# Kernel optimization log

Hardware: AMD Instinct MI355X
Metric: run time of the kernel (lower is better)

## Reference

```python
import jax, jax.numpy as jnp
import numpy as np

D_MODEL = 1024
N_HEADS = 16
D_HEAD = D_MODEL // N_HEADS


def setup_inputs() -> dict:
    key = jax.random.key(0)
    k1, k2, k3 = jax.random.split(key, 3)
    x = jax.random.normal(k1, (4, 2048, D_MODEL), dtype=jnp.float32)
    # nn.Linear weights stored [out, in]; we keep that convention.
    s = 1.0 / np.sqrt(D_MODEL)
    W_qkv = jax.random.uniform(k2, (3 * D_MODEL, D_MODEL), dtype=jnp.float32, minval=-s, maxval=s)
    W_out = jax.random.uniform(k3, (D_MODEL, D_MODEL), dtype=jnp.float32, minval=-s, maxval=s)
    return {"x": x, "W_qkv": W_qkv, "W_out": W_out}


def reference(x, W_qkv, W_out):
    B, T, C = x.shape
    qkv = jnp.einsum('btc,oc->bto', x, W_qkv)  # [B,T,3C]
    q, k, v = jnp.split(qkv, 3, axis=-1)

    def split_heads(t):
        return t.reshape(B, T, N_HEADS, D_HEAD).transpose(0, 2, 1, 3)  # [B,H,T,Dh]

    q, k, v = split_heads(q), split_heads(k), split_heads(v)
    scale = D_HEAD ** -0.5
    scores = jnp.einsum('bhqd,bhkd->bhqk', q, k) * scale  # [B,H,T,T]
    mask = jnp.triu(jnp.ones((T, T), dtype=bool), k=1)
    scores = jnp.where(mask, -jnp.inf, scores)
    att = jax.nn.softmax(scores, axis=-1)
    out = jnp.einsum('bhqk,bhkd->bhqd', att, v)
    out = out.transpose(0, 2, 1, 3).reshape(B, T, C)
    return jnp.einsum('btc,oc->bto', out, W_out)
```

## Files before the change

### kernel.cpp

```cpp
#include <hip/hip_runtime.h>
#include <hip/hip_bf16.h>
#include <math.h>


typedef __attribute__((ext_vector_type(8))) short bf16x8;
typedef __attribute__((ext_vector_type(4))) float f32x4;

__device__ __forceinline__ void async16(const void* g, void* l) {
    __builtin_amdgcn_global_load_lds((const __attribute__((address_space(1))) void*)g,
                                     (__attribute__((address_space(3))) void*)l,
                                     16, 0, 0);
}

__device__ __forceinline__ unsigned short f2b(float f) {
    __hip_bfloat16 h = __float2bfloat16(f);
    return *(unsigned short*)&h;
}

__device__ __forceinline__ unsigned int packbf2(float a, float b) {
    __hip_bfloat162 h2 = __float22bfloat162_rn(make_float2(a, b));
    return *(unsigned int*)&h2;
}

__global__ __launch_bounds__(256)
void cast3_f32_bf16(const float* __restrict__ a, unsigned short* __restrict__ oa, int na,
                    const float* __restrict__ b, unsigned short* __restrict__ ob, int nb,
                    const float* __restrict__ c, unsigned short* __restrict__ oc, int nc)
{
    const int bid  = blockIdx.x;
    const int na_b = na >> 11;
    const int nb_b = nb >> 11;
    const float* in;
    unsigned short* out;
    int base;
    if (bid < na_b)             { in = a; out = oa; base = bid; }
    else if (bid < na_b + nb_b) { in = b; out = ob; base = bid - na_b; }
    else                        { in = c; out = oc; base = bid - na_b - nb_b; }
    int i = (base * 256 + threadIdx.x) * 8;
    float4 x = *(const float4*)(in + i);
    float4 y = *(const float4*)(in + i + 4);
    __hip_bfloat16 r[8];
    r[0] = __float2bfloat16(x.x); r[1] = __float2bfloat16(x.y);
    r[2] = __float2bfloat16(x.z); r[3] = __float2bfloat16(x.w);
    r[4] = __float2bfloat16(y.x); r[5] = __float2bfloat16(y.y);
    r[6] = __float2bfloat16(y.z); r[7] = __float2bfloat16(y.w);
    *(float4*)(out + i) = *(float4*)r;
}

#define BAR8 __builtin_amdgcn_s_barrier()
#define LGKM_PIN(n) do { asm volatile("s_waitcnt lgkmcnt(" #n ")" ::: "memory"); \
                         __builtin_amdgcn_sched_barrier(0); } while (0)
#define VMCNT_PIN(n) do { asm volatile("s_waitcnt vmcnt(" #n ")" ::: "memory"); \
                          __builtin_amdgcn_sched_barrier(0); } while (0)

#define LOAD_A_HALF(B_, QM) do { \
    _Pragma("unroll") \
    for (int mi = 0; mi < 4; ++mi) { \
        af[(QM)*4+mi][0] = *(const bf16x8*)&smem[(B_)*16384 + baseA0 + ((QM)*4+mi)*1024]; \
        af[(QM)*4+mi][1] = *(const bf16x8*)&smem[(B_)*16384 + baseA1 + ((QM)*4+mi)*1024]; \
    } } while (0)

#define LOAD_B2(B_, QN) do { \
    _Pragma("unroll") \
    for (int ni = 0; ni < 2; ++ni) { \
        bf[ni][0] = *(const bf16x8*)&smem[(B_)*16384 + baseB0 + ((QN)*2+ni)*1024]; \
        bf[ni][1] = *(const bf16x8*)&smem[(B_)*16384 + baseB1 + ((QN)*2+ni)*1024]; \
    } } while (0)

#define MFMA16(QM, QN) do { \
    _Pragma("unroll") \
    for (int mi = 0; mi < 4; ++mi) { \
        _Pragma("unroll") \
        for (int ni = 0; ni < 2; ++ni) { \
            acc[(QM)*4+mi][(QN)*2+ni] = __builtin_amdgcn_mfma_f32_16x16x32_bf16( \
                af[(QM)*4+mi][0], bf[ni][0], acc[(QM)*4+mi][(QN)*2+ni], 0, 0, 0); \
            acc[(QM)*4+mi][(QN)*2+ni] = __builtin_amdgcn_mfma_f32_16x16x32_bf16( \
                af[(QM)*4+mi][1], bf[ni][1], acc[(QM)*4+mi][(QN)*2+ni], 0, 0, 0); \
        } } } while (0)

#define STAGE_A8(B_, H_, T_) do { \
    const unsigned short* g_ = A + (size_t)(m0 + (H_)*128) * K + (T_)*64; \
    async16(g_ + g0, &smem[(B_)*16384 + (H_)*8192 + lds0]); \
    async16(g_ + g1, &smem[(B_)*16384 + (H_)*8192 + lds1]); } while (0)

#define STAGE_B8(B_, H_, T_) do { \
    const unsigned short* g_ = Bt + (size_t)(n0 + (H_)*128) * K + (T_)*64; \
    async16(g_ + g0, &smem[32768 + (B_)*16384 + (H_)*8192 + lds0]); \
    async16(g_ + g1, &smem[32768 + (B_)*16384 + (H_)*8192 + lds1]); } while (0)

__global__ __launch_bounds__(512, 2)
void gemm_bf16_nt_8ph(const unsigned short* __restrict__ A,
                      const unsigned short* __restrict__ Bt,
                      unsigned short* __restrict__ C,
                      unsigned short* __restrict__ Vt, int vofs,
                      int M, int N, int K, int sc_ncols, float sc)
{
    __shared__ unsigned short smem[65536];

    const int tid  = threadIdx.x;
    const int lane = tid & 63;
    const int wave = tid >> 6;
    const int wm   = wave >> 2;
    const int wn   = wave & 3;
    const int fr   = lane & 15;
    const int q    = lane >> 4;

    const int ntn = N >> 8;
    int wg = blockIdx.x;
    const int nwg = gridDim.x;
    if ((nwg & 7) == 0) {
        const int cpx = nwg >> 3;
        wg = (wg & 7) * cpx + (wg >> 3);
    }
    const int m0 = (wg / ntn) << 8;
    const int n0 = (wg % ntn) << 8;

    const int c0 = tid, c1 = 512 + tid;
    const int r0 = c0 >> 3, r1 = c1 >> 3;
    const int g0 = r0 * K + (((c0 & 7) ^ (r0 & 7)) << 3);
    const int g1 = r1 * K + (((c1 & 7) ^ (r1 & 7)) << 3);
    const int lds0 = wave * 512;
    const int lds1 = 4096 + wave * 512;

    const int baseA0 = (wm*128 + fr) * 64 + (((0) | q) ^ (fr & 7)) * 8;
    const int baseA1 = (wm*128 + fr) * 64 + (((4) | q) ^ (fr & 7)) * 8;
    const int baseB0 = 32768 + (wn*64 + fr) * 64 + (((0) | q) ^ (fr & 7)) * 8;
    const int baseB1 = 32768 + (wn*64 + fr) * 64 + (((4) | q) ^ (fr & 7)) * 8;

    f32x4 acc[8][4];
#pragma unroll
    for (int i = 0; i < 8; ++i)
#pragma unroll
        for (int j = 0; j < 4; ++j) acc[i][j] = (f32x4){0.f, 0.f, 0.f, 0.f};

    bf16x8 af[8][2];
    bf16x8 bf[2][2];

    STAGE_A8(0, 0, 0); STAGE_A8(0, 1, 0); STAGE_B8(0, 0, 0); STAGE_B8(0, 1, 0);
    STAGE_A8(1, 0, 1); STAGE_A8(1, 1, 1);
    VMCNT_PIN(4);
    BAR8;

    const int niter = K >> 7;
#pragma unroll 1
    for (int i = 0; i < niter; ++i) {
        const int t1 = 2*i + 1, t2 = 2*i + 2, t3 = 2*i + 3;
        const bool st = (i < niter - 1);

        LOAD_A_HALF(0, 0); LOAD_B2(0, 0);
        STAGE_B8(1, 0, t1);
        LGKM_PIN(8);
        BAR8; LGKM_PIN(0);
        __builtin_amdgcn_s_setprio(1); MFMA16(0, 0); __builtin_amdgcn_s_setprio(0);
        BAR8;

        LOAD_A_HALF(0, 1);
        STAGE_B8(1, 1, t1);
        BAR8; LGKM_PIN(0);
        __builtin_amdgcn_s_setprio(1); MFMA16(1, 0); __builtin_amdgcn_s_setprio(0);
        BAR8;

        LOAD_B2(0, 1);
        if (st) STAGE_A8(0, 0, t2);
        BAR8; LGKM_PIN(0);
        __builtin_amdgcn_s_setprio(1); MFMA16(0, 1); __builtin_amdgcn_s_setprio(0);
        BAR8;

        if (st) STAGE_A8(0, 1, t2);
        BAR8;
        __builtin_amdgcn_s_setprio(1); MFMA16(1, 1); __builtin_amdgcn_s_setprio(0);
        if (st) { VMCNT_PIN(4); } else { VMCNT_PIN(0); }
        BAR8;

        LOAD_A_HALF(1, 0); LOAD_B2(1, 0);
        if (st) STAGE_B8(0, 0, t2);
        LGKM_PIN(8);
        BAR8; LGKM_PIN(0);
        __builtin_amdgcn_s_setprio(1); MFMA16(0, 0); __builtin_amdgcn_s_setprio(0);
        BAR8;

        LOAD_A_HALF(1, 1);
        if (st) STAGE_B8(0, 1, t2);
        BAR8; LGKM_PIN(0);
        __builtin_amdgcn_s_setprio(1); MFMA16(1, 0); __builtin_amdgcn_s_setprio(0);
        BAR8;

        LOAD_B2(1, 1);
        if (st) STAGE_A8(1, 0, t3);
        BAR8; LGKM_PIN(0);
        __builtin_amdgcn_s_setprio(1); MFMA16(0, 1); __builtin_amdgcn_s_setprio(0);
        BAR8;

        if (st) STAGE_A8(1, 1, t3);
        BAR8;
        __builtin_amdgcn_s_setprio(1); MFMA16(1, 1); __builtin_amdgcn_s_setprio(0);
        if (st) VMCNT_PIN(4);
        BAR8;
    }

    const int ccol  = n0 + wn * 64 + fr;
    const int crow0 = m0 + wm * 128 + q * 4;

    if (Vt != nullptr && n0 >= vofs) {
        const int hbase = (n0 - vofs) >> 6;
        const int bI = m0 >> 11;
        const int t0g = m0 & 2047;

        __syncthreads();
        {
            const int xw = fr & 7;
            const int csub = (q & 1) * 4;
#pragma unroll
            for (int ni = 0; ni < 4; ++ni) {
                unsigned short* rowp = &smem[(wn * 64 + fr + ni * 16) * 256];
#pragma unroll
                for (int mi = 0; mi < 8; ++mi) {
                    const int c = wm * 16 + mi * 2 + (q >> 1);
                    uint2 pk;
                    pk.x = packbf2(acc[mi][ni][0], acc[mi][ni][1]);
                    pk.y = packbf2(acc[mi][ni][2], acc[mi][ni][3]);
                    *(uint2*)&rowp[((c ^ xw) << 3) + csub] = pk;
                }
            }
        }
        __syncthreads();
        {
            const int j  = lane & 15;
            const int rl = lane >> 4;
#pragma unroll
            for (int it = 0; it < 8; ++it) {
                const int R  = wave * 32 + rl * 8 + it;
                const int xr = R & 7;
                unsigned short* gp = Vt
                    + ((size_t)(bI * 16 + hbase + (R >> 6)) * 64 + (R & 63)) * 2048
                    + t0g;
#pragma unroll
                for (int hh = 0; hh < 2; ++hh) {
                    const int c = hh * 16 + j;
                    float4 v = *(const float4*)&smem[R * 256 + ((c ^ xr) << 3)];
                    *(float4*)(gp + c * 8) = v;
                }
            }
        }
    } else {
#pragma unroll
        for (int mi = 0; mi < 8; ++mi) {
#pragma unroll
            for (int r = 0; r < 4; ++r) {
                const size_t row = (size_t)(crow0 + mi * 16 + r);
#pragma unroll
                for (int ni = 0; ni < 4; ++ni) {
                    float mult = (ccol + ni * 16 < sc_ncols) ? sc : 1.0f;
                    C[row * N + ccol + ni * 16] = f2b(acc[mi][ni][r] * mult);
                }
            }
        }
    }
}

#define MN_LOAD_A_HALF(B_, QM) do { \
    _Pragma("unroll") \
    for (int mi = 0; mi < 4; ++mi) { \
        af[(QM)*4+mi][0] = *(const bf16x8*)&smem[(B_)*16384 + baseA0 + ((QM)*4+mi)*1024]; \
        af[(QM)*4+mi][1] = *(const bf16x8*)&smem[(B_)*16384 + baseA1 + ((QM)*4+mi)*1024]; \
    } } while (0)

#define MN_LOAD_B_NI(B_, NI) do { \
    bf[NI][0] = *(const bf16x8*)&smem[(B_)*8192 + baseB0 + (NI)*1024]; \
    bf[NI][1] = *(const bf16x8*)&smem[(B_)*8192 + baseB1 + (NI)*1024]; } while (0)

#define MN_MFMA8(QM, QN) do { \
    _Pragma("unroll") \
    for (int mi = 0; mi < 4; ++mi) { \
        acc[(QM)*4+mi][QN] = __builtin_amdgcn_mfma_f32_16x16x32_bf16( \
            af[(QM)*4+mi][0], bf[QN][0], acc[(QM)*4+mi][QN], 0, 0, 0); \
        acc[(QM)*4+mi][QN] = __builtin_amdgcn_mfma_f32_16x16x32_bf16( \
            af[(QM)*4+mi][1], bf[QN][1], acc[(QM)*4+mi][QN], 0, 0, 0); \
    } } while (0)

#define MN_STAGE_A(B_, H_, T_) do { \
    const unsigned short* g_ = A + (size_t)(m0 + (H_)*128) * K + (T_)*64; \
    async16(g_ + g0, &smem[(B_)*16384 + (H_)*8192 + lds0]); \
    async16(g_ + g1, &smem[(B_)*16384 + (H_)*8192 + lds1]); } while (0)

#define MN_STAGE_B(B_, T_) do { \
    const unsigned short* g_ = Bt + (size_t)n0 * K + (T_)*64; \
    async16(g_ + g0, &smem[32768 + (B_)*8192 + lds0]); \
    async16(g_ + g1, &smem[32768 + (B_)*8192 + lds1]); } while (0)

template <typename OutT>
__global__ __launch_bounds__(512, 2)
void gemm_bf16_nt_mn(const unsigned short* __restrict__ A,
                     const unsigned short* __restrict__ Bt,
                     OutT* __restrict__ C,
                     int M, int N, int K, int sc_ncols, float sc)
{
    __shared__ unsigned short smem[49152];

    const int tid  = threadIdx.x;
    const int lane = tid & 63;
    const int wave = tid >> 6;
    const int wm   = wave >> 2;
    const int wn   = wave & 3;
    const int fr   = lane & 15;
    const int q    = lane >> 4;

    const int ntn = N >> 7;
    int wg = blockIdx.x;
    const int nwg = gridDim.x;
    if ((nwg & 7) == 0) {
        const int cpx = nwg >> 3;
        wg = (wg & 7) * cpx + (wg >> 3);
    }
    const int m0 = (wg / ntn) << 8;
    const int n0 = (wg % ntn) << 7;

    const int c0 = tid, c1 = 512 + tid;
    const int r0 = c0 >> 3, r1 = c1 >> 3;
    const int g0 = r0 * K + (((c0 & 7) ^ (r0 & 7)) << 3);
    const int g1 = r1 * K + (((c1 & 7) ^ (r1 & 7)) << 3);
    const int lds0 = wave * 512;
    const int lds1 = 4096 + wave * 512;

    const int baseA0 = (wm*128 + fr) * 64 + (((0) | q) ^ (fr & 7)) * 8;
    const int baseA1 = (wm*128 + fr) * 64 + (((4) | q) ^ (fr & 7)) * 8;
    const int baseB0 = 32768 + (wn*32 + fr) * 64 + (((0) | q) ^ (fr & 7)) * 8;
    const int baseB1 = 32768 + (wn*32 + fr) * 64 + (((4) | q) ^ (fr & 7)) * 8;

    f32x4 acc[8][2];
#pragma unroll
    for (int i = 0; i < 8; ++i)
#pragma unroll
        for (int j = 0; j < 2; ++j) acc[i][j] = (f32x4){0.f, 0.f, 0.f, 0.f};

    bf16x8 af[8][2];
    bf16x8 bf[2][2];

    MN_STAGE_A(0, 0, 0); MN_STAGE_A(0, 1, 0); MN_STAGE_B(0, 0);
    MN_STAGE_A(1, 0, 1); MN_STAGE_A(1, 1, 1);
    VMCNT_PIN(4);
    BAR8;

    const int niter = K >> 7;
#pragma unroll 1
    for (int i = 0; i < niter; ++i) {
        const int t1 = 2*i + 1, t2 = 2*i + 2, t3 = 2*i + 3;
        const bool st = (i < niter - 1);

        MN_LOAD_A_HALF(0, 0); MN_LOAD_B_NI(0, 0);
        MN_STAGE_B(1, t1);
        BAR8; LGKM_PIN(0);
        __builtin_amdgcn_s_setprio(1); MN_MFMA8(0, 0); __builtin_amdgcn_s_setprio(0);
        BAR8;

        MN_LOAD_A_HALF(0, 1);
        BAR8; LGKM_PIN(0);
        __builtin_amdgcn_s_setprio(1); MN_MFMA8(1, 0); __builtin_amdgcn_s_setprio(0);
        BAR8;

        MN_LOAD_B_NI(0, 1);
        if (st) MN_STAGE_A(0, 0, t2);
        BAR8; LGKM_PIN(0);
        __builtin_amdgcn_s_setprio(1); MN_MFMA8(0, 1); __builtin_amdgcn_s_setprio(0);
        BAR8;

        if (st) MN_STAGE_A(0, 1, t2);
        BAR8;
        __builtin_amdgcn_s_setprio(1); MN_MFMA8(1, 1); __builtin_amdgcn_s_setprio(0);
        if (st) { VMCNT_PIN(4); } else { VMCNT_PIN(0); }
        BAR8;

        MN_LOAD_A_HALF(1, 0); MN_LOAD_B_NI(1, 0);
        if (st) MN_STAGE_B(0, t2);
        BAR8; LGKM_PIN(0);
        __builtin_amdgcn_s_setprio(1); MN_MFMA8(0, 0); __builtin_amdgcn_s_setprio(0);
        BAR8;

        MN_LOAD_A_HALF(1, 1);
        BAR8; LGKM_PIN(0);
        __builtin_amdgcn_s_setprio(1); MN_MFMA8(1, 0); __builtin_amdgcn_s_setprio(0);
        BAR8;

        MN_LOAD_B_NI(1, 1);
        if (st) MN_STAGE_A(1, 0, t3);
        BAR8; LGKM_PIN(0);
        __builtin_amdgcn_s_setprio(1); MN_MFMA8(0, 1); __builtin_amdgcn_s_setprio(0);
        BAR8;

        if (st) MN_STAGE_A(1, 1, t3);
        BAR8;
        __builtin_amdgcn_s_setprio(1); MN_MFMA8(1, 1); __builtin_amdgcn_s_setprio(0);
        if (st) VMCNT_PIN(4);
        BAR8;
    }

    const int ccol  = n0 + wn * 32 + fr;
    const int crow0 = m0 + wm * 128 + q * 4;
#pragma unroll
    for (int mi = 0; mi < 8; ++mi) {
#pragma unroll
        for (int r = 0; r < 4; ++r) {
            const size_t row = (size_t)(crow0 + mi * 16 + r);
#pragma unroll
            for (int ni = 0; ni < 2; ++ni) {
                float mult = (ccol + ni * 16 < sc_ncols) ? sc : 1.0f;
                float v = acc[mi][ni][r] * mult;
                if constexpr (__is_same(OutT, float)) {
                    C[row * N + ccol + ni * 16] = v;
                } else {
                    C[row * N + ccol + ni * 16] = f2b(v);
                }
            }
        }
    }
}

__global__ __launch_bounds__(256, 4)
void attn_mfma(const unsigned short* __restrict__ qkv,
               const unsigned short* __restrict__ vt,
               unsigned short* __restrict__ out, int T)
{
    __shared__ unsigned short Ks[64 * 64];
    __shared__ unsigned short Vts[64 * 64];
    __shared__ unsigned short Ps[2][64 * 64];

    const int tid  = threadIdx.x;
    const int lane = tid & 63;
    const int wave = tid >> 6;
    const int lc   = lane & 15;
    const int quad = lane >> 4;
    const int nq   = T >> 6;
    const int bid  = blockIdx.x;
    const int bh   = bid & 63;
    const int a    = bid >> 6;
    const int b    = bh >> 4;
    const int h    = bh & 15;
    int qt[2];
    qt[0] = nq - 1 - a;
    qt[1] = a;
    const size_t C3 = 3072;
    const unsigned short* qb  = qkv + (size_t)b * T * C3 + h * 64;
    const unsigned short* kb  = qb + 1024;
    const unsigned short* vtb = vt + (size_t)(b * 16 + h) * 64 * T;

    const int sr  = tid >> 2;
    const int sc  = (tid & 3) * 16;
    const int sw0 = (((tid & 3) * 2)     ^ (sr & 7)) * 8;
    const int sw1 = (((tid & 3) * 2 + 1) ^ (sr & 7)) * 8;

    const int x7  = lc & 7;
    const int rq0 = (quad       ^ x7) * 8;
    const int rq1 = ((quad | 4) ^ x7) * 8;

    const int pq_hi = quad >> 1;
    const int pq_lo = (quad & 1) * 4;

    const int qrow = wave * 16 + lc;
    bf16x8 qf[2][2];
#pragma unroll
    for (int t = 0; t < 2; ++t) {
        const unsigned short* gq = qb + (size_t)(qt[t] * 64 + qrow) * C3 + quad * 8;
        qf[t][0] = *(const bf16x8*)gq;
        qf[t][1] = *(const bf16x8*)(gq + 32);
    }

    f32x4 o_[2][4];
    float l_[2];
#pragma unroll
    for (int t = 0; t < 2; ++t) {
        l_[t] = 0.f;
#pragma unroll
        for (int i = 0; i < 4; ++i) o_[t][i] = (f32x4){0.f, 0.f, 0.f, 0.f};
    }

    const float MB = 8.0f;

    for (int kt = 0; kt <= qt[0]; ++kt) {
        const int k0 = kt * 64;
        const unsigned short* gk = kb + (size_t)(k0 + sr) * C3 + sc;
        float4 kv0 = *(const float4*)gk;
        float4 kv1 = *(const float4*)(gk + 8);
        const unsigned short* gv = vtb + (size_t)sr * T + k0 + sc;
        float4 vv0 = *(const float4*)gv;
        float4 vv1 = *(const float4*)(gv + 8);

        __syncthreads();
        *(float4*)&Ks[sr * 64 + sw0]  = kv0;
        *(float4*)&Ks[sr * 64 + sw1]  = kv1;
        *(float4*)&Vts[sr * 64 + sw0] = vv0;
        *(float4*)&Vts[sr * 64 + sw1] = vv1;
        __syncthreads();

        bf16x8 ak[4][2];
#pragma unroll
        for (int mi = 0; mi < 4; ++mi) {
            ak[mi][0] = *(const bf16x8*)&Ks[(mi * 16 + lc) * 64 + rq0];
            ak[mi][1] = *(const bf16x8*)&Ks[(mi * 16 + lc) * 64 + rq1];
        }

#pragma unroll
        for (int t = 0; t < 2; ++t) {
            if (t == 1 && kt > qt[1]) break;
            f32x4 s[4];
            __builtin_amdgcn_s_setprio(1);
#pragma unroll
            for (int mi = 0; mi < 4; ++mi) {
                s[mi] = (f32x4){0.f, 0.f, 0.f, 0.f};
                s[mi] = __builtin_amdgcn_mfma_f32_16x16x32_bf16(ak[mi][0], qf[t][0], s[mi], 0, 0, 0);
                s[mi] = __builtin_amdgcn_mfma_f32_16x16x32_bf16(ak[mi][1], qf[t][1], s[mi], 0, 0, 0);
            }
            __builtin_amdgcn_s_setprio(0);
            if (kt == qt[t]) {
                const int qg = qt[t] * 64 + wave * 16 + lc;
                const int kbase = k0 + quad * 4;
#pragma unroll
                for (int mi = 0; mi < 4; ++mi)
#pragma unroll
                    for (int r = 0; r < 4; ++r)
                        if (kbase + mi * 16 + r > qg)
                            s[mi][r] = -__builtin_inff();
            }
            float lacc = 0.f;
            const int prow = (wave * 16 + lc) * 64;
#pragma unroll
            for (int mi = 0; mi < 4; ++mi) {
                float p0 = __builtin_amdgcn_exp2f(s[mi][0] - MB);
                float p1 = __builtin_amdgcn_exp2f(s[mi][1] - MB);
                float p2 = __builtin_amdgcn_exp2f(s[mi][2] - MB);
                float p3 = __builtin_amdgcn_exp2f(s[mi][3] - MB);
                lacc += (p0 + p1) + (p2 + p3);
                uint2 pk;
                pk.x = packbf2(p0, p1);
                pk.y = packbf2(p2, p3);
                const int poff = prow + (((2 * mi + pq_hi) ^ x7) * 8) + pq_lo;
                *(uint2*)&Ps[t][poff] = pk;
            }
            l_[t] += lacc;
        }

        bf16x8 av[4][2];
#pragma unroll
        for (int mi = 0; mi < 4; ++mi) {
            av[mi][0] = *(const bf16x8*)&Vts[(mi * 16 + lc) * 64 + rq0];
            av[mi][1] = *(const bf16x8*)&Vts[(mi * 16 + lc) * 64 + rq1];
        }

#pragma unroll
        for (int t = 0; t < 2; ++t) {
            if (t == 1 && kt > qt[1]) break;
            const int prow = (wave * 16 + lc) * 64;
            bf16x8 bp0 = *(const bf16x8*)&Ps[t][prow + rq0];
            bf16x8 bp1 = *(const bf16x8*)&Ps[t][prow + rq1];
            __builtin_amdgcn_s_setprio(1);
#pragma unroll
            for (int mi = 0; mi < 4; ++mi) {
                o_[t][mi] = __builtin_amdgcn_mfma_f32_16x16x32_bf16(av[mi][0], bp0, o_[t][mi], 0, 0, 0);
                o_[t][mi] = __builtin_amdgcn_mfma_f32_16x16x32_bf16(av[mi][1], bp1, o_[t][mi], 0, 0, 0);
            }
            __builtin_amdgcn_s_setprio(0);
        }
    }

#pragma unroll
    for (int t = 0; t < 2; ++t) {
        float rs = l_[t];
        rs += __shfl_xor(rs, 16);
        rs += __shfl_xor(rs, 32);
        float inv = 1.f / rs;
        unsigned short* ob = out + ((size_t)b * T + qt[t] * 64 + wave * 16 + lc) * 1024
                           + h * 64 + quad * 4;
#pragma unroll
        for (int mi = 0; mi < 4; ++mi) {
            uint2 pk;
            pk.x = packbf2(o_[t][mi][0] * inv, o_[t][mi][1] * inv);
            pk.y = packbf2(o_[t][mi][2] * inv, o_[t][mi][3] * inv);
            *(uint2*)(ob + mi * 16) = pk;
        }
    }
}

extern "C" void kernel_launch(void* const* d_in, const int* in_sizes, int n_in,
                              void* d_out, int out_size, void* d_ws, size_t ws_size,
                              hipStream_t stream)
{
    const float* x     = (const float*)d_in[0];
    const float* W_qkv = (const float*)d_in[1];
    const float* W_out = (const float*)d_in[2];
    float* out = (float*)d_out;

    const int C = 1024;
    const int T = 2048;
    const int M = in_sizes[0] / C;
    const int B = M / T;
    const int n_x    = in_sizes[0];
    const int n_wqkv = in_sizes[1];
    const int n_wout = in_sizes[2];

    unsigned short* x_bf    = (unsigned short*)d_ws;
    unsigned short* wqkv_bf = x_bf    + n_x;
    unsigned short* wout_bf = wqkv_bf + n_wqkv;
    unsigned short* qkv_bf  = wout_bf + n_wout;
    unsigned short* vt_bf   = qkv_bf  + (size_t)M * 3 * C;
    unsigned short* ao_bf   = vt_bf   + (size_t)B * 16 * 64 * T;

    cast3_f32_bf16<<<(n_x + n_wqkv + n_wout) / 2048, 256, 0, stream>>>(
        x, x_bf, n_x, W_qkv, wqkv_bf, n_wqkv, W_out, wout_bf, n_wout);

    const float QSC = 0.18033688011112042f;
    gemm_bf16_nt_8ph<<<dim3(((3*C) / 256) * (M / 256)), 512, 0, stream>>>(
        x_bf, wqkv_bf, qkv_bf, vt_bf, 2*C, M, 3*C, C, C, QSC);

    const int nq = T / 64;
    attn_mfma<<<dim3(B * 16 * (nq / 2)), 256, 0, stream>>>(qkv_bf, vt_bf, ao_bf, T);

    gemm_bf16_nt_mn<float><<<dim3((C/128) * (M/256)), 512, 0, stream>>>(
        ao_bf, wout_bf, out, M, C, C, 0, 1.0f);
}
```

Before: 231.0 us.

## Double-buffer K/V tiles in attention with async global-to-LDS loads

Replaces the synchronous register-staged K/V tile load in the causal attention kernel with double-buffered LDS tiles filled by global_load_lds, so the next tile is prefetched while the current one is computed. This removes the two barriers and the register round trip each iteration and overlaps memory latency with the MFMA work. It doubles K/V LDS use, which may reduce occupancy under the 4-block launch bound, and it relies on the VMCNT_PIN macro and on the swizzle being consistent with the readers.

Result: slower. 248.2 us (+7.4%).

```diff
diff --git a/kernel.cpp b/kernel.cpp
--- a/kernel.cpp
+++ b/kernel.cpp
@@ -420,8 +420,8 @@
                const unsigned short* __restrict__ vt,
                unsigned short* __restrict__ out, int T)
 {
-    __shared__ unsigned short Ks[64 * 64];
-    __shared__ unsigned short Vts[64 * 64];
+    __shared__ unsigned short Ks[2][64 * 64];
+    __shared__ unsigned short Vts[2][64 * 64];
     __shared__ unsigned short Ps[2][64 * 64];
 
     const int tid  = threadIdx.x;
@@ -443,10 +443,9 @@
     const unsigned short* kb  = qb + 1024;
     const unsigned short* vtb = vt + (size_t)(b * 16 + h) * 64 * T;
 
-    const int sr  = tid >> 2;
-    const int sc  = (tid & 3) * 16;
-    const int sw0 = (((tid & 3) * 2)     ^ (sr & 7)) * 8;
-    const int sw1 = (((tid & 3) * 2 + 1) ^ (sr & 7)) * 8;
+    const int srow_c0 = wave * 16 + (lane >> 3);
+    const int gcS     = ((lane & 7) ^ (lane >> 3)) * 8;
+    const int ldsW    = wave * 1024;
 
     const int x7  = lc & 7;
     const int rq0 = (quad       ^ x7) * 8;
@@ -474,28 +473,34 @@
     }
 
     const float MB = 8.0f;
-
-    for (int kt = 0; kt <= qt[0]; ++kt) {
-        const int k0 = kt * 64;
-        const unsigned short* gk = kb + (size_t)(k0 + sr) * C3 + sc;
-        float4 kv0 = *(const float4*)gk;
-        float4 kv1 = *(const float4*)(gk + 8);
-        const unsigned short* gv = vtb + (size_t)sr * T + k0 + sc;
-        float4 vv0 = *(const float4*)gv;
-        float4 vv1 = *(const float4*)(gv + 8);
-
-        __syncthreads();
-        *(float4*)&Ks[sr * 64 + sw0]  = kv0;
-        *(float4*)&Ks[sr * 64 + sw1]  = kv1;
-        *(float4*)&Vts[sr * 64 + sw0] = vv0;
-        *(float4*)&Vts[sr * 64 + sw1] = vv1;
-        __syncthreads();
+    const int qt0 = qt[0];
+
+#define ATTN_STAGE_KV(BUF, KT) do { \
+    const int k0s = (KT) * 64; \
+    _Pragma("unroll") \
+    for (int c = 0; c < 2; ++c) { \
+        const int srw = srow_c0 + c * 8; \
+        async16(kb + (size_t)(k0s + srw) * C3 + gcS, &Ks[BUF][ldsW + c * 512]); \
+        async16(vtb + (size_t)srw * T + k0s + gcS,   &Vts[BUF][ldsW + c * 512]); \
+    } } while (0)
+
+    ATTN_STAGE_KV(0, 0);
+    VMCNT_PIN(0);
+    __syncthreads();
+
+    for (int kt = 0; kt <= qt0; ++kt) {
+        const int k0  = kt * 64;
+        const int cur = kt & 1;
+        const unsigned short* Kc = Ks[cur];
+        const unsigned short* Vc = Vts[cur];
+
+        if (kt < qt0) ATTN_STAGE_KV(cur ^ 1, kt + 1);
 
         bf16x8 ak[4][2];
 #pragma unroll
         for (int mi = 0; mi < 4; ++mi) {
-            ak[mi][0] = *(const bf16x8*)&Ks[(mi * 16 + lc) * 64 + rq0];
-            ak[mi][1] = *(const bf16x8*)&Ks[(mi * 16 + lc) * 64 + rq1];
+            ak[mi][0] = *(const bf16x8*)&Kc[(mi * 16 + lc) * 64 + rq0];
+            ak[mi][1] = *(const bf16x8*)&Kc[(mi * 16 + lc) * 64 + rq1];
         }
 
 #pragma unroll
@@ -541,8 +546,8 @@
         bf16x8 av[4][2];
 #pragma unroll
         for (int mi = 0; mi < 4; ++mi) {
-            av[mi][0] = *(const bf16x8*)&Vts[(mi * 16 + lc) * 64 + rq0];
-            av[mi][1] = *(const bf16x8*)&Vts[(mi * 16 + lc) * 64 + rq1];
+            av[mi][0] = *(const bf16x8*)&Vc[(mi * 16 + lc) * 64 + rq0];
+            av[mi][1] = *(const bf16x8*)&Vc[(mi * 16 + lc) * 64 + rq1];
         }
 
 #pragma unroll
@@ -559,7 +564,13 @@
             }
             __builtin_amdgcn_s_setprio(0);
         }
-    }
+
+        if (kt < qt0) {
+            VMCNT_PIN(0);
+            __syncthreads();
+        }
+    }
+#undef ATTN_STAGE_KV
 
 #pragma unroll
     for (int t = 0; t < 2; ++t) {
```
